# Optimization experiments

Hardware: AMD Instinct MI355X
Metric: run time of the kernel (lower is better)

Reference implementation:

```python
import jax, jax.numpy as jnp
import numpy as np

N_HEADS = 12


def setup_inputs() -> dict:
    key = jax.random.key(0)
    ks = jax.random.split(key, 3)
    B, N, C = 32, 1024, 768
    x = jax.random.normal(ks[0], (B, N, C), dtype=jnp.float32)
    w_qkv = jax.random.normal(ks[1], (C, 3 * C), dtype=jnp.float32) * (1.0 / np.sqrt(C))
    b_qkv = jnp.zeros((3 * C,), dtype=jnp.float32)
    w_out = jax.random.normal(ks[2], (C, C), dtype=jnp.float32) * (1.0 / np.sqrt(C))
    b_out = jnp.zeros((C,), dtype=jnp.float32)
    return {"x": x, "w_qkv": w_qkv, "b_qkv": b_qkv, "w_out": w_out, "b_out": b_out}


def reference(x, w_qkv, b_qkv, w_out, b_out):
    B, N, C = x.shape
    H = N_HEADS
    D = C // H  # head_dim
    qkv = (x @ w_qkv + b_qkv).reshape(B, N, 3, H, D)
    qkv = jnp.transpose(qkv, (2, 0, 3, 1, 4))
    q, k, v = qkv[0], qkv[1], qkv[2]
    # channel attention: k^T @ v -> (B,H,D,D), scaled by sqrt(head_dim)
    attn = jnp.einsum("bhnd,bhne->bhde", k, v) / np.sqrt(D).astype(np.float32)
    attn = jax.nn.softmax(attn, axis=-1)
    # attn @ q^T -> (B,H,D,N); swapaxes -> (B,H,N,D)
    out = jnp.einsum("bhde,bhne->bhnd", attn, q)
    # ProjOut: merge heads (B,N,C) + Dense(C)
    out = jnp.transpose(out, (0, 2, 1, 3)).reshape(B, N, C)
    return out @ w_out + b_out
```

## Files before the change

### kernel.cpp

```cpp
#include <hip/hip_runtime.h>
#include <hip/hip_bf16.h>
#include <stdint.h>
#include <stddef.h>

#define B_ 32
#define N_ 1024
#define C_ 768
#define H_ 12
#define D_ 64
#define M_ (B_*N_)
#define TC_ (3*C_)

typedef __bf16 bf16_t;
typedef __attribute__((ext_vector_type(8))) __bf16 bf16x8;
typedef __attribute__((ext_vector_type(4))) __bf16 bf16x4;
typedef __attribute__((ext_vector_type(4))) float  f32x4;

#define MFMA16(a,b,c) __builtin_amdgcn_mfma_f32_16x16x32_bf16(a,b,c,0,0,0)

__device__ __forceinline__ void lds_load16(const void* g, void* l) {
  __builtin_amdgcn_global_load_lds(
      (const __attribute__((address_space(1))) void*)g,
      (__attribute__((address_space(3))) void*)l, 16, 0, 0);
}

__global__ void cvt_bf16(const float* __restrict__ in, bf16_t* __restrict__ out, int n) {
  int i = (blockIdx.x * 256 + threadIdx.x) * 8;
  if (i >= n) return;
  const float4 a = *(const float4*)(in + i);
  const float4 b = *(const float4*)(in + i + 4);
  bf16x8 r;
  r[0]=(bf16_t)a.x; r[1]=(bf16_t)a.y; r[2]=(bf16_t)a.z; r[3]=(bf16_t)a.w;
  r[4]=(bf16_t)b.x; r[5]=(bf16_t)b.y; r[6]=(bf16_t)b.z; r[7]=(bf16_t)b.w;
  *(bf16x8*)(out + i) = r;
}

__global__ void transpose_cvt(const float* __restrict__ in, bf16_t* __restrict__ out,
                              int R, int Cc) {
  __shared__ float t[32][33];
  const int c0 = blockIdx.x * 32, r0 = blockIdx.y * 32;
  const int tx = threadIdx.x & 31, ty = threadIdx.x >> 5;
  #pragma unroll
  for (int k = 0; k < 4; ++k)
    t[ty + k*8][tx] = in[(size_t)(r0 + ty + k*8)*Cc + c0 + tx];
  __syncthreads();
  #pragma unroll
  for (int k = 0; k < 4; ++k)
    out[(size_t)(c0 + ty + k*8)*R + r0 + tx] = (bf16_t)t[tx][ty + k*8];
}

template<int MODE>
__global__ __launch_bounds__(512, 2)
void gemm_bt(const bf16_t* __restrict__ A, const bf16_t* __restrict__ BT,
             const float* __restrict__ bias, float* __restrict__ Cout,
             bf16_t* __restrict__ qh,
             bf16_t* __restrict__ kthi, bf16_t* __restrict__ vthi,
             int nbx)
{
  __shared__ __align__(16) char smem[131072];

  const int nwg = gridDim.x;
  const int cpx = nwg >> 3;
  const int bid = blockIdx.x;
  const int swz = (bid & 7) * cpx + (bid >> 3);
  const int bx  = swz % nbx;
  const int by  = swz / nbx;

  const int tid  = threadIdx.x;
  const int wave = tid >> 6;
  const int lane = tid & 63;
  const int rowBase = by * 256;
  const int colBase = bx * 256;
  const int wr = wave >> 2;
  const int wc = wave & 3;
  const int fr  = lane & 15;
  const int fob = (lane >> 4) * 16;
  const int b   = rowBase >> 10;
  const int nn0 = rowBase & (N_ - 1);

  const int srow = tid >> 2;
  const int scol = (tid & 3) * 8;
  const bf16_t *Ap0, *Ap1, *Bp0, *Bp1;
  if (MODE == 3) {
    Ap0 = A + (size_t)b * (H_*N_*D_) + (size_t)(nn0 + srow) * D_ + scol;
    Ap1 = Ap0 + (size_t)128 * D_;
    const size_t bts = (size_t)b * C_ * C_;
    Bp0 = BT + bts + (size_t)(colBase + srow) * 768 + scol;
    Bp1 = Bp0 + (size_t)128 * 768;
  } else {
    Ap0 = A + (size_t)(rowBase + srow) * 768 + scol;
    Ap1 = Ap0 + (size_t)128 * 768;
    Bp0 = BT + (size_t)(colBase + srow) * 768 + scol;
    Bp1 = Bp0 + (size_t)128 * 768;
  }

  const int aoff = (wr*128 + fr)*64 + fob;
  const int boff = 16384 + (wc*64 + fr)*64 + fob;

#define RDA(BI,MM) (*(const bf16x8*)(smem + (BI)*32768 + aoff + (MM)*1024))
#define RDB(BI,NN) (*(const bf16x8*)(smem + (BI)*32768 + boff + (NN)*1024))

#define A_OFF(K0) ((MODE == 3) ? ((size_t)((K0) >> 6) << 16) + ((K0) & 32) : (size_t)(K0))

#define STAGE_A(BI, T) do {                                                   \
    const int k0_ = (T) * 32;                                                 \
    const size_t ao_ = A_OFF(k0_);                                            \
    lds_load16(Ap0 + ao_, smem + (BI)*32768 + tid*16);                        \
    lds_load16(Ap1 + ao_, smem + (BI)*32768 + 8192 + tid*16);                 \
  } while (0)

#define STAGE_B(BI, T) do {                                                   \
    const int k0_ = (T) * 32;                                                 \
    lds_load16(Bp0 + k0_, smem + (BI)*32768 + 16384 + tid*16);                \
    lds_load16(Bp1 + k0_, smem + (BI)*32768 + 24576 + tid*16);                \
  } while (0)

  f32x4 acc[8][4];
  #pragma unroll
  for (int m = 0; m < 8; ++m)
    #pragma unroll
    for (int n = 0; n < 4; ++n) acc[m][n] = f32x4{0.f,0.f,0.f,0.f};

#define TILE(BI, T, DOST, VM) do {                                            \
    asm volatile("s_waitcnt vmcnt(" #VM ")" ::: "memory");                    \
    __builtin_amdgcn_sched_barrier(0);                                        \
    __builtin_amdgcn_s_barrier();                                             \
    __builtin_amdgcn_sched_barrier(0);                                        \
    if (DOST) STAGE_A(((BI)+3)&3, (T)+3);                                     \
    bf16x8 b0_=RDB(BI,0), b1_=RDB(BI,1), b2_=RDB(BI,2), b3_=RDB(BI,3);        \
    bf16x8 a0_=RDA(BI,0), a1_=RDA(BI,1), a2_=RDA(BI,2), a3_=RDA(BI,3);        \
    __builtin_amdgcn_s_setprio(1);                                            \
    acc[0][0]=MFMA16(a0_,b0_,acc[0][0]); acc[0][1]=MFMA16(a0_,b1_,acc[0][1]); \
    acc[0][2]=MFMA16(a0_,b2_,acc[0][2]); acc[0][3]=MFMA16(a0_,b3_,acc[0][3]); \
    acc[1][0]=MFMA16(a1_,b0_,acc[1][0]); acc[1][1]=MFMA16(a1_,b1_,acc[1][1]); \
    acc[1][2]=MFMA16(a1_,b2_,acc[1][2]); acc[1][3]=MFMA16(a1_,b3_,acc[1][3]); \
    acc[2][0]=MFMA16(a2_,b0_,acc[2][0]); acc[2][1]=MFMA16(a2_,b1_,acc[2][1]); \
    acc[2][2]=MFMA16(a2_,b2_,acc[2][2]); acc[2][3]=MFMA16(a2_,b3_,acc[2][3]); \
    acc[3][0]=MFMA16(a3_,b0_,acc[3][0]); acc[3][1]=MFMA16(a3_,b1_,acc[3][1]); \
    acc[3][2]=MFMA16(a3_,b2_,acc[3][2]); acc[3][3]=MFMA16(a3_,b3_,acc[3][3]); \
    __builtin_amdgcn_s_setprio(0);                                            \
    if (DOST) STAGE_B(((BI)+3)&3, (T)+3);                                     \
    a0_=RDA(BI,4); a1_=RDA(BI,5); a2_=RDA(BI,6); a3_=RDA(BI,7);               \
    __builtin_amdgcn_s_setprio(1);                                            \
    acc[4][0]=MFMA16(a0_,b0_,acc[4][0]); acc[4][1]=MFMA16(a0_,b1_,acc[4][1]); \
    acc[4][2]=MFMA16(a0_,b2_,acc[4][2]); acc[4][3]=MFMA16(a0_,b3_,acc[4][3]); \
    acc[5][0]=MFMA16(a1_,b0_,acc[5][0]); acc[5][1]=MFMA16(a1_,b1_,acc[5][1]); \
    acc[5][2]=MFMA16(a1_,b2_,acc[5][2]); acc[5][3]=MFMA16(a1_,b3_,acc[5][3]); \
    acc[6][0]=MFMA16(a2_,b0_,acc[6][0]); acc[6][1]=MFMA16(a2_,b1_,acc[6][1]); \
    acc[6][2]=MFMA16(a2_,b2_,acc[6][2]); acc[6][3]=MFMA16(a2_,b3_,acc[6][3]); \
    acc[7][0]=MFMA16(a3_,b0_,acc[7][0]); acc[7][1]=MFMA16(a3_,b1_,acc[7][1]); \
    acc[7][2]=MFMA16(a3_,b2_,acc[7][2]); acc[7][3]=MFMA16(a3_,b3_,acc[7][3]); \
    __builtin_amdgcn_s_setprio(0);                                            \
    asm volatile("s_waitcnt lgkmcnt(0)" ::: "memory");                        \
    __builtin_amdgcn_sched_barrier(0);                                        \
  } while (0)

  STAGE_A(0,0); STAGE_B(0,0);
  STAGE_A(1,1); STAGE_B(1,1);
  STAGE_A(2,2); STAGE_B(2,2);

  #pragma unroll 1
  for (int t = 0; t < 20; t += 4) {
    TILE(0, t,   1, 8);
    TILE(1, t+1, 1, 8);
    TILE(2, t+2, 1, 8);
    TILE(3, t+3, 1, 8);
  }
  TILE(0, 20, 1, 8);
  TILE(1, 21, 0, 8);
  TILE(2, 22, 0, 4);
  TILE(3, 23, 0, 0);

#undef TILE
#undef STAGE_A
#undef STAGE_B
#undef A_OFF
#undef RDA
#undef RDB

  if (MODE == 3) {
    #pragma unroll
    for (int n = 0; n < 4; ++n) {
      const int gc = colBase + wc*64 + n*16 + fr;
      const float bb = bias[gc];
      #pragma unroll
      for (int m = 0; m < 8; ++m) {
        const int gr = rowBase + wr*128 + m*16 + ((lane >> 4) << 2);
        #pragma unroll
        for (int j = 0; j < 4; ++j)
          Cout[(size_t)(gr + j)*C_ + gc] = acc[m][n][j] + bb;
      }
    }
  } else {
    __syncthreads();
    bf16_t* tile = (bf16_t*)smem;
    const int s = colBase / C_;
    #pragma unroll
    for (int ch = 0; ch < 2; ++ch) {
      if (ch) __syncthreads();
      if ((wc >> 1) == ch) {
        #pragma unroll
        for (int n = 0; n < 4; ++n) {
          const int cl = (wc & 1)*64 + n*16 + fr;
          const float bb = bias[colBase + ch*128 + cl];
          #pragma unroll
          for (int m = 0; m < 8; ++m) {
            const int r0 = wr*128 + m*16 + ((lane >> 4) << 2);
            bf16x4 hv;
            hv[0]=(bf16_t)(acc[m][n][0]+bb); hv[1]=(bf16_t)(acc[m][n][1]+bb);
            hv[2]=(bf16_t)(acc[m][n][2]+bb); hv[3]=(bf16_t)(acc[m][n][3]+bb);
            *(bf16x4*)&tile[cl*260 + r0] = hv;
          }
        }
      }
      __syncthreads();
      if (s == 0) {
        const int r = tid >> 1, hh = tid & 1;
        const int h = (colBase >> 6) + ch*2 + hh;
        bf16_t* dst = qh + (((size_t)b*H_ + h)*N_ + nn0 + r)*D_;
        #pragma unroll
        for (int i0 = 0; i0 < 64; i0 += 8) {
          bf16x8 vv;
          #pragma unroll
          for (int i = 0; i < 8; ++i) vv[i] = tile[(hh*64 + i0 + i)*260 + r];
          *(bf16x8*)&dst[i0] = vv;
        }
      } else {
        const int c = tid >> 2, rq = tid & 3;
        const int rem = colBase + ch*128 + c - s*C_;
        const int h = rem >> 6, d = rem & 63;
        bf16_t* dst = (s == 1 ? kthi : vthi)
                      + (((size_t)b*H_ + h)*D_ + d)*N_ + nn0 + rq*64;
        #pragma unroll
        for (int i0 = 0; i0 < 64; i0 += 8)
          *(bf16x8*)&dst[i0] = *(const bf16x8*)&tile[c*260 + rq*64 + i0];
      }
    }
  }
}

__global__ __launch_bounds__(256, 2)
void attn_softmax_k(const bf16_t* __restrict__ kthi, const bf16_t* __restrict__ vthi,
                    bf16_t* __restrict__ attnT)
{
  __shared__ float tile[64][65];
  __shared__ float invs[64];
  const int bh = blockIdx.x;
  const int tid = threadIdx.x, wave = tid >> 6, lane = tid & 63;
  const int fr = lane & 15, fo = (lane >> 4) * 8;
  const size_t base = (size_t)bh * D_ * N_;
  f32x4 acc[4][4] = {{0.f,0.f,0.f,0.f}};
  const int k0lo = wave * 256;
  #pragma unroll 1
  for (int k0 = k0lo; k0 < k0lo + 256; k0 += 32) {
    bf16x8 ah[4], bhv[4];
    #pragma unroll
    for (int m = 0; m < 4; ++m)
      ah[m] = *(const bf16x8*)&kthi[base + (size_t)(m*16 + fr)*N_ + k0 + fo];
    #pragma unroll
    for (int n = 0; n < 4; ++n)
      bhv[n] = *(const bf16x8*)&vthi[base + (size_t)(n*16 + fr)*N_ + k0 + fo];
    #pragma unroll
    for (int m = 0; m < 4; ++m)
      #pragma unroll
      for (int n = 0; n < 4; ++n)
        acc[m][n] = MFMA16(ah[m], bhv[n], acc[m][n]);
  }
  for (int w = 0; w < 4; ++w) {
    if (wave == w) {
      #pragma unroll
      for (int m = 0; m < 4; ++m)
        #pragma unroll
        for (int n = 0; n < 4; ++n) {
          const int row = m*16 + ((lane >> 4) << 2);
          const int col = n*16 + fr;
          #pragma unroll
          for (int j = 0; j < 4; ++j) {
            if (w == 0) tile[row+j][col]  = acc[m][n][j];
            else        tile[row+j][col] += acc[m][n][j];
          }
        }
    }
    __syncthreads();
  }
  if (tid < 64) {
    float mx = -3.0e38f;
    #pragma unroll
    for (int c = 0; c < 64; ++c) mx = fmaxf(mx, tile[tid][c]);
    mx *= 0.125f;
    float ssum = 0.f;
    #pragma unroll
    for (int c = 0; c < 64; ++c) {
      const float ev = __expf(tile[tid][c]*0.125f - mx);
      tile[tid][c] = ev;
      ssum += ev;
    }
    invs[tid] = 1.0f / ssum;
  }
  __syncthreads();
  if (tid < 64) {
    bf16_t* ao = attnT + (size_t)bh * D_ * D_ + tid * D_;
    #pragma unroll
    for (int d0 = 0; d0 < 64; d0 += 8) {
      bf16x8 vv;
      #pragma unroll
      for (int i = 0; i < 8; ++i) vv[i] = (bf16_t)(tile[d0+i][tid] * invs[d0+i]);
      *(bf16x8*)&ao[d0] = vv;
    }
  }
}

__global__ __launch_bounds__(256, 2)
void compose_w2(const bf16_t* __restrict__ woutT, const bf16_t* __restrict__ attnT,
                bf16_t* __restrict__ w2t)
{
  const int jb = blockIdx.x;
  const int bh = blockIdx.y;
  const int b = bh / H_, h = bh - b*H_;
  const int tid = threadIdx.x, wave = tid >> 6, lane = tid & 63;
  const int fr = lane & 15, fo = (lane >> 4) * 8;
  const bf16_t* at = attnT + (size_t)bh * D_ * D_;
  f32x4 acc[2][4] = {{0.f,0.f,0.f,0.f}};
  #pragma unroll
  for (int kk = 0; kk < 2; ++kk) {
    bf16x8 af[2], bfv[4];
    #pragma unroll
    for (int m = 0; m < 2; ++m)
      af[m] = *(const bf16x8*)&woutT[(size_t)(jb*128 + wave*32 + m*16 + fr)*C_ + h*64 + kk*32 + fo];
    #pragma unroll
    for (int n = 0; n < 4; ++n)
      bfv[n] = *(const bf16x8*)&at[(n*16 + fr)*64 + kk*32 + fo];
    #pragma unroll
    for (int m = 0; m < 2; ++m)
      #pragma unroll
      for (int n = 0; n < 4; ++n)
        acc[m][n] = MFMA16(af[m], bfv[n], acc[m][n]);
  }
  bf16_t* wb = w2t + (size_t)b * C_ * C_;
  #pragma unroll
  for (int m = 0; m < 2; ++m) {
    const int j = jb*128 + wave*32 + m*16 + ((lane >> 4) << 2);
    #pragma unroll
    for (int n = 0; n < 4; ++n) {
      const int e = n*16 + fr;
      #pragma unroll
      for (int jj = 0; jj < 4; ++jj)
        wb[(size_t)(j + jj)*C_ + h*64 + e] = (bf16_t)acc[m][n][jj];
    }
  }
}

extern "C" void kernel_launch(void* const* d_in, const int* in_sizes, int n_in,
                              void* d_out, int out_size, void* d_ws, size_t ws_size,
                              hipStream_t stream)
{
  (void)in_sizes; (void)n_in; (void)out_size;
  const float* x     = (const float*)d_in[0];
  const float* w_qkv = (const float*)d_in[1];
  const float* b_qkv = (const float*)d_in[2];
  const float* w_out = (const float*)d_in[3];
  const float* b_out = (const float*)d_in[4];
  float* out = (float*)d_out;

  const size_t sz_xb   = (size_t)M_*C_*2;
  const size_t sz_wq   = (size_t)TC_*C_*2;
  const size_t sz_wo   = (size_t)C_*C_*2;
  const size_t sz_qh   = (size_t)B_*H_*N_*D_*2;
  const size_t sz_kv   = (size_t)B_*H_*D_*N_*2;
  const size_t sz_attn = (size_t)B_*H_*D_*D_*2;

  char* p = (char*)d_ws;
  bf16_t* xb    = (bf16_t*)p; p += sz_xb;
  bf16_t* wqkvT = (bf16_t*)p; p += sz_wq;
  bf16_t* woutT = (bf16_t*)p; p += sz_wo;
  bf16_t* qh    = (bf16_t*)p; p += sz_qh;
  bf16_t* kthi  = (bf16_t*)p; p += sz_kv;
  bf16_t* vthi  = (bf16_t*)p; p += sz_kv;
  bf16_t* attnT = (bf16_t*)p; p += sz_attn;
  const size_t base_need = (size_t)(p - (char*)d_ws);
  bf16_t* w2t = xb;

  if (ws_size < base_need) return;

  cvt_bf16<<<dim3((M_*C_)/2048), 256, 0, stream>>>(x, xb, M_*C_);
  transpose_cvt<<<dim3(TC_/32, C_/32), 256, 0, stream>>>(w_qkv, wqkvT, C_, TC_);
  transpose_cvt<<<dim3(C_/32,  C_/32), 256, 0, stream>>>(w_out, woutT, C_, C_);

  gemm_bt<1><<<dim3((TC_/256)*(M_/256)), 512, 0, stream>>>(
      xb, wqkvT, b_qkv, nullptr, qh, kthi, vthi, TC_/256);

  attn_softmax_k<<<dim3(B_*H_), 256, 0, stream>>>(kthi, vthi, attnT);

  compose_w2<<<dim3(C_/128, B_*H_), 256, 0, stream>>>(woutT, attnT, w2t);

  gemm_bt<3><<<dim3((C_/256)*(M_/256)), 512, 0, stream>>>(
      qh, w2t, b_out, out, nullptr, nullptr, nullptr, C_/256);
}
```

Before: 307.1 us.

## Restructure GEMM main loop to BK=64 double buffering with XOR-swizzled LDS

Replaces the 4-stage, K=32 LDS ring with a 2-stage, K=64 double buffer. Each tile is split into four sub-phases that interleave global-to-LDS staging with MFMA rows, and the LDS layout uses an XOR swizzle to avoid bank conflicts on fragment reads. The epilogue now writes 64-column chunks in four rounds instead of two 128-column rounds. The aim is fewer barriers per unit of K and conflict-free LDS reads. In exchange it adds more intra-tile barriers, a full vmcnt(0) wait on every tile and less prefetch depth.

```diff
diff --git a/kernel.cpp b/kernel.cpp
--- a/kernel.cpp
+++ b/kernel.cpp
@@ -73,47 +73,42 @@
   const int colBase = bx * 256;
   const int wr = wave >> 2;
   const int wc = wave & 3;
-  const int fr  = lane & 15;
-  const int fob = (lane >> 4) * 16;
+  const int fr = lane & 15;
+  const int hi = lane >> 4;
   const int b   = rowBase >> 10;
   const int nn0 = rowBase & (N_ - 1);
 
-  const int srow = tid >> 2;
-  const int scol = (tid & 3) * 8;
-  const bf16_t *Ap0, *Ap1, *Bp0, *Bp1;
-  if (MODE == 3) {
-    Ap0 = A + (size_t)b * (H_*N_*D_) + (size_t)(nn0 + srow) * D_ + scol;
-    Ap1 = Ap0 + (size_t)128 * D_;
-    const size_t bts = (size_t)b * C_ * C_;
-    Bp0 = BT + bts + (size_t)(colBase + srow) * 768 + scol;
-    Bp1 = Bp0 + (size_t)128 * 768;
-  } else {
-    Ap0 = A + (size_t)(rowBase + srow) * 768 + scol;
-    Ap1 = Ap0 + (size_t)128 * 768;
-    Bp0 = BT + (size_t)(colBase + srow) * 768 + scol;
-    Bp1 = Bp0 + (size_t)128 * 768;
-  }
-
-  const int aoff = (wr*128 + fr)*64 + fob;
-  const int boff = 16384 + (wc*64 + fr)*64 + fob;
-
-#define RDA(BI,MM) (*(const bf16x8*)(smem + (BI)*32768 + aoff + (MM)*1024))
-#define RDB(BI,NN) (*(const bf16x8*)(smem + (BI)*32768 + boff + (NN)*1024))
-
-#define A_OFF(K0) ((MODE == 3) ? ((size_t)((K0) >> 6) << 16) + ((K0) & 32) : (size_t)(K0))
-
-#define STAGE_A(BI, T) do {                                                   \
-    const int k0_ = (T) * 32;                                                 \
-    const size_t ao_ = A_OFF(k0_);                                            \
-    lds_load16(Ap0 + ao_, smem + (BI)*32768 + tid*16);                        \
-    lds_load16(Ap1 + ao_, smem + (BI)*32768 + 8192 + tid*16);                 \
-  } while (0)
-
-#define STAGE_B(BI, T) do {                                                   \
-    const int k0_ = (T) * 32;                                                 \
-    lds_load16(Bp0 + k0_, smem + (BI)*32768 + 16384 + tid*16);                \
-    lds_load16(Bp1 + k0_, smem + (BI)*32768 + 24576 + tid*16);                \
-  } while (0)
+  const int srowL = tid >> 3;
+  const int scol  = (((tid & 7) ^ ((tid >> 3) & 7)) << 3);
+  const size_t AKS = (MODE == 3) ? (size_t)65536 : (size_t)64;
+  const size_t ABS = (MODE == 3) ? (size_t)4096  : (size_t)49152;
+  const bf16_t* Abase;
+  if (MODE == 3)
+    Abase = A + (size_t)b*(H_*N_*D_) + (size_t)(nn0 + srowL)*D_ + scol;
+  else
+    Abase = A + (size_t)(rowBase + srowL)*768 + scol;
+  const size_t bts = (MODE == 3) ? (size_t)b*C_*C_ : 0;
+  const bf16_t* Bbase = BT + bts + (size_t)(colBase + srowL)*768 + scol;
+
+  const int chx0 = (( hi     ) ^ (fr & 7)) << 4;
+  const int chx1 = ((4 + hi  ) ^ (fr & 7)) << 4;
+  const int arow = (wr*128 + fr) * 128;
+  const int brow = 32768 + (wc*64 + fr) * 128;
+
+#define RA(BUF,M,CX) (*(const bf16x8*)(smem + (BUF) + arow + (M)*2048 + (CX)))
+#define RB(BUF,N,CX) (*(const bf16x8*)(smem + (BUF) + brow + (N)*2048 + (CX)))
+#define SA(BUF,T,BLK) lds_load16(Abase + (size_t)(T)*AKS + (size_t)(BLK)*ABS, \
+                                 smem + (BUF) + (BLK)*8192 + tid*16)
+#define SB(BUF,T,BLK) lds_load16(Bbase + (size_t)(T)*64 + (size_t)(BLK)*49152, \
+                                 smem + (BUF) + 32768 + (BLK)*8192 + tid*16)
+
+#define BARX() do { __builtin_amdgcn_sched_barrier(0); \
+                    __builtin_amdgcn_s_barrier(); \
+                    __builtin_amdgcn_sched_barrier(0); } while (0)
+#define LGKM0() do { asm volatile("s_waitcnt lgkmcnt(0)" ::: "memory"); \
+                     __builtin_amdgcn_sched_barrier(0); } while (0)
+#define VM0()   do { asm volatile("s_waitcnt vmcnt(0)" ::: "memory"); \
+                     __builtin_amdgcn_sched_barrier(0); } while (0)
 
   f32x4 acc[8][4];
   #pragma unroll
@@ -121,62 +116,70 @@
     #pragma unroll
     for (int n = 0; n < 4; ++n) acc[m][n] = f32x4{0.f,0.f,0.f,0.f};
 
-#define TILE(BI, T, DOST, VM) do {                                            \
-    asm volatile("s_waitcnt vmcnt(" #VM ")" ::: "memory");                    \
-    __builtin_amdgcn_sched_barrier(0);                                        \
-    __builtin_amdgcn_s_barrier();                                             \
-    __builtin_amdgcn_sched_barrier(0);                                        \
-    if (DOST) STAGE_A(((BI)+3)&3, (T)+3);                                     \
-    bf16x8 b0_=RDB(BI,0), b1_=RDB(BI,1), b2_=RDB(BI,2), b3_=RDB(BI,3);        \
-    bf16x8 a0_=RDA(BI,0), a1_=RDA(BI,1), a2_=RDA(BI,2), a3_=RDA(BI,3);        \
-    __builtin_amdgcn_s_setprio(1);                                            \
-    acc[0][0]=MFMA16(a0_,b0_,acc[0][0]); acc[0][1]=MFMA16(a0_,b1_,acc[0][1]); \
-    acc[0][2]=MFMA16(a0_,b2_,acc[0][2]); acc[0][3]=MFMA16(a0_,b3_,acc[0][3]); \
-    acc[1][0]=MFMA16(a1_,b0_,acc[1][0]); acc[1][1]=MFMA16(a1_,b1_,acc[1][1]); \
-    acc[1][2]=MFMA16(a1_,b2_,acc[1][2]); acc[1][3]=MFMA16(a1_,b3_,acc[1][3]); \
-    acc[2][0]=MFMA16(a2_,b0_,acc[2][0]); acc[2][1]=MFMA16(a2_,b1_,acc[2][1]); \
-    acc[2][2]=MFMA16(a2_,b2_,acc[2][2]); acc[2][3]=MFMA16(a2_,b3_,acc[2][3]); \
-    acc[3][0]=MFMA16(a3_,b0_,acc[3][0]); acc[3][1]=MFMA16(a3_,b1_,acc[3][1]); \
-    acc[3][2]=MFMA16(a3_,b2_,acc[3][2]); acc[3][3]=MFMA16(a3_,b3_,acc[3][3]); \
-    __builtin_amdgcn_s_setprio(0);                                            \
-    if (DOST) STAGE_B(((BI)+3)&3, (T)+3);                                     \
-    a0_=RDA(BI,4); a1_=RDA(BI,5); a2_=RDA(BI,6); a3_=RDA(BI,7);               \
-    __builtin_amdgcn_s_setprio(1);                                            \
-    acc[4][0]=MFMA16(a0_,b0_,acc[4][0]); acc[4][1]=MFMA16(a0_,b1_,acc[4][1]); \
-    acc[4][2]=MFMA16(a0_,b2_,acc[4][2]); acc[4][3]=MFMA16(a0_,b3_,acc[4][3]); \
-    acc[5][0]=MFMA16(a1_,b0_,acc[5][0]); acc[5][1]=MFMA16(a1_,b1_,acc[5][1]); \
-    acc[5][2]=MFMA16(a1_,b2_,acc[5][2]); acc[5][3]=MFMA16(a1_,b3_,acc[5][3]); \
-    acc[6][0]=MFMA16(a2_,b0_,acc[6][0]); acc[6][1]=MFMA16(a2_,b1_,acc[6][1]); \
-    acc[6][2]=MFMA16(a2_,b2_,acc[6][2]); acc[6][3]=MFMA16(a2_,b3_,acc[6][3]); \
-    acc[7][0]=MFMA16(a3_,b0_,acc[7][0]); acc[7][1]=MFMA16(a3_,b1_,acc[7][1]); \
-    acc[7][2]=MFMA16(a3_,b2_,acc[7][2]); acc[7][3]=MFMA16(a3_,b3_,acc[7][3]); \
-    __builtin_amdgcn_s_setprio(0);                                            \
-    asm volatile("s_waitcnt lgkmcnt(0)" ::: "memory");                        \
-    __builtin_amdgcn_sched_barrier(0);                                        \
+#define MROW(M,AK0,AK1)                                                        \
+    acc[M][0]=MFMA16(AK0,b0a,acc[M][0]); acc[M][0]=MFMA16(AK1,b0b,acc[M][0]);  \
+    acc[M][1]=MFMA16(AK0,b1a,acc[M][1]); acc[M][1]=MFMA16(AK1,b1b,acc[M][1]);  \
+    acc[M][2]=MFMA16(AK0,b2a,acc[M][2]); acc[M][2]=MFMA16(AK1,b2b,acc[M][2]);  \
+    acc[M][3]=MFMA16(AK0,b3a,acc[M][3]); acc[M][3]=MFMA16(AK1,b3b,acc[M][3]);
+
+#define TILE8(BUF,NBUF,T,DOST) do {                                            \
+                         \
+    bf16x8 b0a=RB(BUF,0,chx0), b0b=RB(BUF,0,chx1);                             \
+    bf16x8 b1a=RB(BUF,1,chx0), b1b=RB(BUF,1,chx1);                             \
+    bf16x8 b2a=RB(BUF,2,chx0), b2b=RB(BUF,2,chx1);                             \
+    bf16x8 b3a=RB(BUF,3,chx0), b3b=RB(BUF,3,chx1);                             \
+    bf16x8 a0=RA(BUF,0,chx0), a0k=RA(BUF,0,chx1);                              \
+    bf16x8 a1=RA(BUF,1,chx0), a1k=RA(BUF,1,chx1);                              \
+    if (DOST) { SA(NBUF,(T)+1,0); SA(NBUF,(T)+1,1); SA(NBUF,(T)+1,2); }        \
+    BARX(); LGKM0();                                                           \
+    __builtin_amdgcn_s_setprio(1); MROW(0,a0,a0k) MROW(1,a1,a1k)               \
+    __builtin_amdgcn_s_setprio(0);                                             \
+    BARX();                                                                    \
+                                                                  \
+    a0=RA(BUF,2,chx0); a0k=RA(BUF,2,chx1);                                     \
+    a1=RA(BUF,3,chx0); a1k=RA(BUF,3,chx1);                                     \
+    if (DOST) { SA(NBUF,(T)+1,3); SB(NBUF,(T)+1,0); SB(NBUF,(T)+1,1); }        \
+    BARX(); LGKM0();                                                           \
+    __builtin_amdgcn_s_setprio(1); MROW(2,a0,a0k) MROW(3,a1,a1k)               \
+    __builtin_amdgcn_s_setprio(0);                                             \
+    BARX();                                                                    \
+                                                                  \
+    a0=RA(BUF,4,chx0); a0k=RA(BUF,4,chx1);                                     \
+    a1=RA(BUF,5,chx0); a1k=RA(BUF,5,chx1);                                     \
+    if (DOST) { SB(NBUF,(T)+1,2); SB(NBUF,(T)+1,3); }                          \
+    BARX(); LGKM0();                                                           \
+    __builtin_amdgcn_s_setprio(1); MROW(4,a0,a0k) MROW(5,a1,a1k)               \
+    __builtin_amdgcn_s_setprio(0);                                             \
+    BARX();                                                                    \
+     \
+    a0=RA(BUF,6,chx0); a0k=RA(BUF,6,chx1);                                     \
+    a1=RA(BUF,7,chx0); a1k=RA(BUF,7,chx1);                                     \
+    BARX(); LGKM0();                                                           \
+    __builtin_amdgcn_s_setprio(1); MROW(6,a0,a0k) MROW(7,a1,a1k)               \
+    __builtin_amdgcn_s_setprio(0);                                             \
+    VM0();                                                                     \
+    BARX();                                                                    \
   } while (0)
 
-  STAGE_A(0,0); STAGE_B(0,0);
-  STAGE_A(1,1); STAGE_B(1,1);
-  STAGE_A(2,2); STAGE_B(2,2);
+  SA(0,0,0); SA(0,0,1); SA(0,0,2); SA(0,0,3);
+  SB(0,0,0); SB(0,0,1); SB(0,0,2); SB(0,0,3);
+  VM0();
+  BARX();
 
   #pragma unroll 1
-  for (int t = 0; t < 20; t += 4) {
-    TILE(0, t,   1, 8);
-    TILE(1, t+1, 1, 8);
-    TILE(2, t+2, 1, 8);
-    TILE(3, t+3, 1, 8);
-  }
-  TILE(0, 20, 1, 8);
-  TILE(1, 21, 0, 8);
-  TILE(2, 22, 0, 4);
-  TILE(3, 23, 0, 0);
-
-#undef TILE
-#undef STAGE_A
-#undef STAGE_B
-#undef A_OFF
-#undef RDA
-#undef RDB
+  for (int T = 0; T < 12; ++T) {
+    const int CB = (T & 1) << 16;
+    const int NB = CB ^ 65536;
+    const bool dost = (T < 11);
+    TILE8(CB, NB, T, dost);
+  }
+
+#undef TILE8
+#undef MROW
+#undef RA
+#undef RB
+#undef SA
+#undef SB
 
   if (MODE == 3) {
     #pragma unroll
@@ -195,14 +198,14 @@
     __syncthreads();
     bf16_t* tile = (bf16_t*)smem;
     const int s = colBase / C_;
-    #pragma unroll
-    for (int ch = 0; ch < 2; ++ch) {
+    #pragma unroll 1
+    for (int ch = 0; ch < 4; ++ch) {
       if (ch) __syncthreads();
-      if ((wc >> 1) == ch) {
+      if (wc == ch) {
         #pragma unroll
         for (int n = 0; n < 4; ++n) {
-          const int cl = (wc & 1)*64 + n*16 + fr;
-          const float bb = bias[colBase + ch*128 + cl];
+          const int cl = n*16 + fr;
+          const float bb = bias[colBase + ch*64 + cl];
           #pragma unroll
           for (int m = 0; m < 8; ++m) {
             const int r0 = wr*128 + m*16 + ((lane >> 4) << 2);
@@ -214,29 +217,33 @@
         }
       }
       __syncthreads();
+      const int gcol0 = colBase + ch*64;
       if (s == 0) {
+        const int h = gcol0 >> 6;
         const int r = tid >> 1, hh = tid & 1;
-        const int h = (colBase >> 6) + ch*2 + hh;
-        bf16_t* dst = qh + (((size_t)b*H_ + h)*N_ + nn0 + r)*D_;
+        bf16_t* dst = qh + (((size_t)b*H_ + h)*N_ + nn0 + r)*D_ + hh*32;
         #pragma unroll
-        for (int i0 = 0; i0 < 64; i0 += 8) {
+        for (int i0 = 0; i0 < 32; i0 += 8) {
           bf16x8 vv;
           #pragma unroll
-          for (int i = 0; i < 8; ++i) vv[i] = tile[(hh*64 + i0 + i)*260 + r];
+          for (int i = 0; i < 8; ++i) vv[i] = tile[(hh*32 + i0 + i)*260 + r];
           *(bf16x8*)&dst[i0] = vv;
         }
       } else {
-        const int c = tid >> 2, rq = tid & 3;
-        const int rem = colBase + ch*128 + c - s*C_;
-        const int h = rem >> 6, d = rem & 63;
+        const int rem = gcol0 - s*C_;
+        const int h = rem >> 6;
+        const int d = tid >> 3, nq = (tid & 7)*32;
         bf16_t* dst = (s == 1 ? kthi : vthi)
-                      + (((size_t)b*H_ + h)*D_ + d)*N_ + nn0 + rq*64;
+                      + (((size_t)b*H_ + h)*D_ + d)*N_ + nn0 + nq;
         #pragma unroll
-        for (int i0 = 0; i0 < 64; i0 += 8)
-          *(bf16x8*)&dst[i0] = *(const bf16x8*)&tile[c*260 + rq*64 + i0];
+        for (int i0 = 0; i0 < 32; i0 += 8)
+          *(bf16x8*)&dst[i0] = *(const bf16x8*)&tile[d*260 + nq + i0];
       }
     }
   }
+#undef BARX
+#undef LGKM0
+#undef VM0
 }
 
 __global__ __launch_bounds__(256, 2)
```

New measurement: 311.6 us. About the same (+1.5%).
